# Optimization experiments

Hardware: AMD Instinct MI355X
Metric: run time of the kernel (lower is better)

Reference implementation:

```python
import jax, jax.numpy as jnp
import numpy as np

B = 256      # graphs per batch
N_PER = 256  # nodes per graph
DEG = 16     # avg degree
F_IN = 128   # num_feats
H = 128      # nhid
C = 10       # num_classes
RATIO = 0.5
N = B * N_PER
E = B * N_PER * DEG
K1 = int(np.ceil(RATIO * N_PER))   # 128
K2 = int(np.ceil(RATIO * K1))      # 64
K3 = int(np.ceil(RATIO * K2))      # 32


def setup_inputs() -> dict:
    key = jax.random.key(0)
    ks = jax.random.split(key, 24)
    off = (jnp.arange(B, dtype=jnp.int32) * N_PER)[:, None]
    # random intra-graph edges (block-diagonal adjacency)
    src = (jax.random.randint(ks[0], (B, N_PER * DEG), 0, N_PER, dtype=jnp.int32) + off).reshape(-1)
    dst = (jax.random.randint(ks[1], (B, N_PER * DEG), 0, N_PER, dtype=jnp.int32) + off).reshape(-1)
    x = jax.random.normal(ks[2], (N, F_IN), jnp.float32)

    def glorot(k, fi, fo):
        s = jnp.sqrt(2.0 / (fi + fo)).astype(jnp.float32)
        return jax.random.normal(k, (fi, fo), jnp.float32) * s

    inp = dict(x=x, src=src, dst=dst)
    # GCN conv layers
    inp['W1'] = glorot(ks[3], F_IN, H); inp['b1'] = jnp.zeros((H,), jnp.float32)
    inp['W2'] = glorot(ks[4], H, H);    inp['b2'] = jnp.zeros((H,), jnp.float32)
    inp['W3'] = glorot(ks[5], H, H);    inp['b3'] = jnp.zeros((H,), jnp.float32)
    # SAGPool score layers (GCNConv(nhid, 1))
    inp['Ws1'] = glorot(ks[6], H, 1); inp['bs1'] = jnp.zeros((1,), jnp.float32)
    inp['Ws2'] = glorot(ks[7], H, 1); inp['bs2'] = jnp.zeros((1,), jnp.float32)
    inp['Ws3'] = glorot(ks[8], H, 1); inp['bs3'] = jnp.zeros((1,), jnp.float32)
    # MLP head
    inp['Wl1'] = glorot(ks[9], 2 * H, H);      inp['bl1'] = jnp.zeros((H,), jnp.float32)
    inp['Wl2'] = glorot(ks[10], H, H // 2);    inp['bl2'] = jnp.zeros((H // 2,), jnp.float32)
    inp['Wl3'] = glorot(ks[11], H // 2, C);    inp['bl3'] = jnp.zeros((C,), jnp.float32)
    return inp


def _gcn(x, W, b, src, dst, mask):
    # PyG GCNConv: add self-loops, sym-normalize by deg^-1/2, aggregate x@W.
    # `mask` marks surviving nodes; edges with a dropped endpoint are inactive,
    # which is equivalent to PyG's filter_adj subgraph relabeling.
    emf = (mask[src] & mask[dst]).astype(x.dtype)           # [E]
    deg = jax.ops.segment_sum(emf, dst, num_segments=N) + mask.astype(x.dtype)  # +1 self loop
    dinv = jnp.where(deg > 0, jax.lax.rsqrt(deg), 0.0)
    h = x @ W                                                # [N, out]
    w = emf * dinv[src] * dinv[dst]                          # [E]
    agg = jax.ops.segment_sum(h[src] * w[:, None], dst, num_segments=N)
    agg = agg + h * (dinv * dinv * mask.astype(x.dtype))[:, None]  # self-loop term
    return agg + b


def _sagpool(x, Ws, bs, src, dst, mask, k):
    # score = GCNConv(in,1)(x); keep top-k per graph; x = x[perm]*tanh(score[perm])
    score = _gcn(x, Ws, bs, src, dst, mask)[:, 0]            # [N]
    s = jnp.where(mask, score, -jnp.inf).reshape(B, N_PER)
    idx = jax.lax.top_k(s, k)[1]                             # [B, k]
    nm = jnp.zeros((B, N_PER), bool).at[jnp.arange(B)[:, None], idx].set(True).reshape(-1)
    x = x * jnp.tanh(score)[:, None] * nm[:, None].astype(x.dtype)
    return x, nm


def _readout(x, mask, count):
    # global_max_pool || global_mean_pool over surviving nodes of each graph
    xb = x.reshape(B, N_PER, H)
    mb = mask.reshape(B, N_PER)[:, :, None]
    mx = jnp.max(jnp.where(mb, xb, -jnp.inf), axis=1)
    mn = jnp.sum(xb * mb.astype(x.dtype), axis=1) / jnp.asarray(count, x.dtype)
    return jnp.concatenate([mx, mn], axis=1)                 # [B, 2H]


def reference(x, src, dst, W1, b1, W2, b2, W3, b3, Ws1, bs1, Ws2, bs2, Ws3, bs3,
              Wl1, bl1, Wl2, bl2, Wl3, bl3):
    m0 = jnp.ones((N,), bool)
    h = jax.nn.relu(_gcn(x, W1, b1, src, dst, m0))
    h, m1 = _sagpool(h, Ws1, bs1, src, dst, m0, K1)
    r1 = _readout(h, m1, K1)
    h = jax.nn.relu(_gcn(h, W2, b2, src, dst, m1))
    h, m2 = _sagpool(h, Ws2, bs2, src, dst, m1, K2)
    r2 = _readout(h, m2, K2)
    h = jax.nn.relu(_gcn(h, W3, b3, src, dst, m2))
    h, m3 = _sagpool(h, Ws3, bs3, src, dst, m2, K3)
    r3 = _readout(h, m3, K3)
    z = r1 + r2 + r3                                         # [B, 2H]
    z = jax.nn.relu(z @ Wl1 + bl1)
    # dropout skipped (eval mode / training=False)
    z = jax.nn.relu(z @ Wl2 + bl2)
    return jax.nn.log_softmax(jax.nn.relu(z @ Wl3 + bl3), axis=-1)
```

## Files before the change

kernel.cpp:

```cpp
#include <hip/hip_runtime.h>
#include <math.h>

#define NGRAPH 256
#define NPG 256
#define HF 128
#define EPG 4096
#define EPG2 4352
#define FSTR 132
#define PSTR 136

typedef __attribute__((ext_vector_type(8))) short bf16x8;
typedef __attribute__((ext_vector_type(4))) float f32x4;

template<int N> struct IC { static constexpr int value = N; };
template<bool B> struct BC { static constexpr bool value = B; };

static __device__ __forceinline__ unsigned bcu(float f){ return __builtin_bit_cast(unsigned, f); }
static __device__ __forceinline__ float bcf(unsigned u){ return __builtin_bit_cast(float, u); }
static __device__ __forceinline__ unsigned rtn16(float f){
  unsigned u = bcu(f);
  return (u + 0x7FFFu + ((u >> 16) & 1u)) >> 16;
}

__global__ __launch_bounds__(256) void prep_wt(const float* __restrict__ W1,
                                               const float* __restrict__ W2,
                                               const float* __restrict__ W3,
                                               short* __restrict__ Wt) {
  int idx = blockIdx.x * 256 + threadIdx.x;
  int L = idx >> 14, r = idx & 16383;
  int k = r >> 7, n = r & 127;
  const float* W = (L == 0) ? W1 : (L == 1) ? W2 : W3;
  float w = W[k*128 + n];
  unsigned hi = rtn16(w);
  float lo = w - bcf(hi << 16);
  short* Whi = Wt + (size_t)L * 2 * 16384;
  short* Wlo = Whi + 16384;
  Whi[n*128 + k] = (short)hi;
  Wlo[n*128 + k] = (short)(bcu(lo) >> 16);
}

#define BSTEP(OK, OI, KKc, Jc) do { \
  bool iLess = ((tid & (Jc)) == 0); \
  bool descR = ((tid & (KKc)) == 0); \
  bool myFirst = (kf > (OK)) || (kf == (OK) && ki < (OI)); \
  bool keep = (iLess == descR) ? myFirst : !myFirst; \
  if (!keep) { kf = (OK); ki = (OI); } \
} while (0)

#define WAVE0_SCAN() do { \
  if (wid == 0) { \
    int b4 = lane*4; \
    int c0=cntA[b4+0], c1=cntA[b4+1], c2=cntA[b4+2], c3=cntA[b4+3]; \
    int tot = c0+c1+c2+c3; \
    int run = tot; \
    _Pragma("unroll") \
    for (int off=1; off<64; off<<=1) { \
      int u = __shfl_up(run, off); \
      run += (lane >= off) ? u : 0; \
    } \
    int st = run - tot; \
    rloc[b4+0]=(unsigned short)st; \
    rloc[b4+1]=(unsigned short)(st+c0); \
    rloc[b4+2]=(unsigned short)(st+c0+c1); \
    rloc[b4+3]=(unsigned short)(st+c0+c1+c2); \
    curA[b4+0]=st; curA[b4+1]=st+c0; curA[b4+2]=st+c0+c1; curA[b4+3]=st+c0+c1+c2; \
    if (lane == 63) rloc[NPG] = (unsigned short)run; \
  } \
} while (0)

__global__ __launch_bounds__(1024, 4)
void fused_net(
    const float* __restrict__ x,
    const int* __restrict__ srcI, const int* __restrict__ dstI,
    const short* __restrict__ WtAll,
    const float* __restrict__ b1, const float* __restrict__ Ws1, const float* __restrict__ bs1,
    const float* __restrict__ b2, const float* __restrict__ Ws2, const float* __restrict__ bs2,
    const float* __restrict__ b3, const float* __restrict__ Ws3, const float* __restrict__ bs3,
    const float* __restrict__ Wl1, const float* __restrict__ bl1,
    const float* __restrict__ Wl2, const float* __restrict__ bl2,
    const float* __restrict__ Wl3, const float* __restrict__ bl3,
    float* __restrict__ out)
{
  __shared__ __align__(16) short hpair[2][NPG*PSTR];
  __shared__ unsigned char colS[EPG2 + 8];
  __shared__ unsigned short rloc[NPG+2];
  __shared__ unsigned selM[8];
  __shared__ float dinv[NPG];
  __shared__ __align__(16) float bvec[HF];
  __shared__ __align__(16) float wsv[HF];
  __shared__ float score[NPG];
  __shared__ float tscale[NPG];
  __shared__ float skey[NPG];
  __shared__ int   sidx[NPG];
  __shared__ unsigned char rank8[NPG];
  __shared__ unsigned char lut[NPG];
  __shared__ __align__(16) float red[1024];
  __shared__ __align__(16) float red2[1024];
  __shared__ float zacc[2*HF];

  float* tbufF = (float*)&hpair[0][0];
  short* hp0 = &hpair[0][0];
  short* hp1 = &hpair[1][0];
  int* cntA = (int*)skey;
  int* curA = sidx;

  int tid = threadIdx.x;
  int g = blockIdx.x;
  size_t nbase = (size_t)g * NPG;
  int lane = tid & 63, wid = tid >> 6;

  const float4* X4 = (const float4*)(x + nbase*HF);
  #pragma unroll
  for (int i = 0; i < 8; ++i) {
    int f4 = tid + i*1024;
    int r = f4 >> 5, kq = f4 & 31;
    float4 val = X4[f4];
    unsigned rx = rtn16(val.x), ry = rtn16(val.y), rz = rtn16(val.z), rw = rtn16(val.w);
    uint2 ph; ph.x = rx | (ry << 16); ph.y = rz | (rw << 16);
    float lx = val.x - bcf(rx << 16), ly = val.y - bcf(ry << 16);
    float lz = val.z - bcf(rz << 16), lw = val.w - bcf(rw << 16);
    uint2 pl; pl.x = (bcu(lx) >> 16) | (bcu(ly) & 0xFFFF0000u);
    pl.y = (bcu(lz) >> 16) | (bcu(lw) & 0xFFFF0000u);
    *(uint2*)&hp0[r*PSTR + kq*4] = ph;
    *(uint2*)&hp1[r*PSTR + kq*4] = pl;
  }

  int nb = g * NPG;
  int dloc[4], sloc[4];
  #pragma unroll
  for (int it = 0; it < 4; ++it) {
    int e = g*EPG + tid + it*1024;
    dloc[it] = dstI[e] - nb;
    sloc[it] = srcI[e] - nb;
  }

  if (tid < NPG) { cntA[tid] = 1; lut[tid] = (unsigned char)tid; }
  __syncthreads();
  #pragma unroll
  for (int it = 0; it < 4; ++it) atomicAdd(&cntA[dloc[it]], 1);
  __syncthreads();
  WAVE0_SCAN();
  __syncthreads();
  #pragma unroll
  for (int it = 0; it < 4; ++it) {
    int slot = atomicAdd(&curA[dloc[it]], 1);
    colS[slot] = (unsigned char)sloc[it];
  }
  if (tid < NPG) colS[rloc[tid+1] - 1] = (unsigned char)tid;

  auto run_layer = [&](auto nrc, auto kc, auto firstc, auto packc,
                       const short* Whi, const short* Wlo,
                       const float* bias, const float* Wsc, const float* bscp) {
    constexpr int NR = decltype(nrc)::value;
    constexpr int K  = decltype(kc)::value;
    constexpr bool FIRST = decltype(firstc)::value;
    constexpr bool PACK  = decltype(packc)::value;
    constexpr int TPN = 1024 / NR;
    constexpr int NI  = 32 / TPN;
    constexpr int SH  = (TPN == 4) ? 2 : ((TPN == 8) ? 3 : 4);
    constexpr int RT  = NR / 64;
    int v = tid >> SH, q = tid & (TPN - 1);
    int cb0 = 4 * q;

    __syncthreads();

    if (tid < HF) { bvec[tid] = bias[tid]; wsv[tid] = Wsc[tid]; }
    if (tid < NR) dinv[tid] = 1.0f / sqrtf((float)((int)rloc[tid+1] - (int)rloc[tid]));

    {
      int rg = wid & 3, cg = wid >> 2;
      int lr = lane & 15, lk8 = (lane >> 4) * 8;
      f32x4 tacc[RT][2] = {};
      #pragma unroll
      for (int kc2 = 0; kc2 < 4; ++kc2) {
        int k0 = kc2*32 + lk8;
        bf16x8 ah[RT], al[RT];
        #pragma unroll
        for (int rt = 0; rt < RT; ++rt) {
          int row = rg*(NR/4) + rt*16 + lr;
          ah[rt] = *(const bf16x8*)&hp0[row*PSTR + k0];
          al[rt] = *(const bf16x8*)&hp1[row*PSTR + k0];
        }
        #pragma unroll
        for (int ct = 0; ct < 2; ++ct) {
          int n = cg*32 + ct*16 + lr;
          bf16x8 bh = *(const bf16x8*)&Whi[n*HF + k0];
          bf16x8 bl = *(const bf16x8*)&Wlo[n*HF + k0];
          #pragma unroll
          for (int rt = 0; rt < RT; ++rt) {
            tacc[rt][ct] = __builtin_amdgcn_mfma_f32_16x16x32_bf16(ah[rt], bh, tacc[rt][ct], 0, 0, 0);
            tacc[rt][ct] = __builtin_amdgcn_mfma_f32_16x16x32_bf16(al[rt], bh, tacc[rt][ct], 0, 0, 0);
            tacc[rt][ct] = __builtin_amdgcn_mfma_f32_16x16x32_bf16(ah[rt], bl, tacc[rt][ct], 0, 0, 0);
          }
        }
      }
      __syncthreads();
      #pragma unroll
      for (int rt = 0; rt < RT; ++rt) {
        int row0 = rg*(NR/4) + rt*16 + (lane >> 4)*4;
        float d0 = dinv[row0+0], d1 = dinv[row0+1], d2 = dinv[row0+2], d3 = dinv[row0+3];
        #pragma unroll
        for (int ct = 0; ct < 2; ++ct) {
          int c = cg*32 + ct*16 + (lane & 15);
          tbufF[(row0+0)*FSTR + c] = tacc[rt][ct][0] * d0;
          tbufF[(row0+1)*FSTR + c] = tacc[rt][ct][1] * d1;
          tbufF[(row0+2)*FSTR + c] = tacc[rt][ct][2] * d2;
          tbufF[(row0+3)*FSTR + c] = tacc[rt][ct][3] * d3;
        }
      }
    }
    __syncthreads();

    float4 hv[NI];
    {
      float4 acc[NI];
      #pragma unroll
      for (int j = 0; j < NI; ++j) { acc[j].x = acc[j].y = acc[j].z = acc[j].w = 0.f; }
      int e0 = rloc[v], e1 = rloc[v+1];
      int sA = colS[e0], sB = colS[e0+1], sC = colS[e0+2], sD = colS[e0+3];
      int e = e0;
      for (; e + 1 < e1; e += 2) {
        int s0 = sA, s1 = sB;
        sA = sC; sB = sD; sC = colS[e+4]; sD = colS[e+5];
        const float* g0 = &tbufF[s0*FSTR + cb0];
        const float* g1 = &tbufF[s1*FSTR + cb0];
        #pragma unroll
        for (int j = 0; j < NI; ++j) {
          float4 t0 = *(const float4*)&g0[j*4*TPN];
          float4 t1 = *(const float4*)&g1[j*4*TPN];
          acc[j].x += t0.x + t1.x; acc[j].y += t0.y + t1.y;
          acc[j].z += t0.z + t1.z; acc[j].w += t0.w + t1.w;
        }
      }
      if (e < e1) {
        const float* g0 = &tbufF[sA*FSTR + cb0];
        #pragma unroll
        for (int j = 0; j < NI; ++j) {
          float4 t0 = *(const float4*)&g0[j*4*TPN];
          acc[j].x += t0.x; acc[j].y += t0.y; acc[j].z += t0.z; acc[j].w += t0.w;
        }
      }
      float dv = dinv[v];
      float p = 0.f;
      #pragma unroll
      for (int j = 0; j < NI; ++j) {
        int ci = cb0 + j*4*TPN;
        float4 bv = *(const float4*)&bvec[ci];
        float4 wv = *(const float4*)&wsv[ci];
        float4 a;
        a.x = fmaxf(fmaf(dv, acc[j].x, bv.x), 0.f);
        a.y = fmaxf(fmaf(dv, acc[j].y, bv.y), 0.f);
        a.z = fmaxf(fmaf(dv, acc[j].z, bv.z), 0.f);
        a.w = fmaxf(fmaf(dv, acc[j].w, bv.w), 0.f);
        hv[j] = a;
        p += a.x*wv.x + a.y*wv.y + a.z*wv.z + a.w*wv.w;
      }
      red[tid] = p;
    }
    __syncthreads();
    if (tid < NR) {
      float s4 = 0.f;
      #pragma unroll
      for (int t = 0; t < TPN/4; ++t) {
        float4 qd = *(const float4*)&red[tid*TPN + 4*t];
        s4 += (qd.x + qd.y) + (qd.z + qd.w);
      }
      tscale[tid] = s4 * dinv[tid];
    }
    __syncthreads();
    if (tid < NR) {
      int e0 = rloc[tid], e1 = rloc[tid+1];
      float sa = 0.f;
      int sA = colS[e0], sB = colS[e0+1], sC = colS[e0+2], sD = colS[e0+3];
      for (int e = e0; e < e1; ++e) {
        int s = sA; sA = sB; sB = sC; sC = sD; sD = colS[e+4];
        sa += tscale[s];
      }
      score[tid] = dinv[tid] * sa + bscp[0];
    }
    __syncthreads();

    float kf = -INFINITY; int ki = tid;
    if (tid < NR) {
      kf = score[tid];
      for (int kk = 2; kk <= 64; kk <<= 1)
        for (int j = kk >> 1; j > 0; j >>= 1) {
          float ok = __shfl_xor(kf, j);
          int   oi = __shfl_xor(ki, j);
          BSTEP(ok, oi, kk, j);
        }
    } else if (tid < NR + 8) selM[tid - NR] = 0u;

    if constexpr (NR == 256) {
      if (tid < NR) { skey[tid] = kf; sidx[tid] = ki; }
      __syncthreads();
      if (tid < NR) {
        int l = tid ^ 64; float ok = skey[l]; int oi = sidx[l];
        BSTEP(ok, oi, 128, 64);
        for (int j = 32; j > 0; j >>= 1) {
          float sk = __shfl_xor(kf, j); int si = __shfl_xor(ki, j);
          BSTEP(sk, si, 128, j);
        }
      }
      __syncthreads();
      if (tid < NR) { skey[tid] = kf; sidx[tid] = ki; }
      __syncthreads();
      if (tid < NR) {
        int l = tid ^ 128; float ok = skey[l]; int oi = sidx[l];
        BSTEP(ok, oi, 256, 128);
      }
      __syncthreads();
      if (tid < NR) { skey[tid] = kf; sidx[tid] = ki; }
      __syncthreads();
      if (tid < NR) {
        int l = tid ^ 64; float ok = skey[l]; int oi = sidx[l];
        BSTEP(ok, oi, 256, 64);
        for (int j = 32; j > 0; j >>= 1) {
          float sk = __shfl_xor(kf, j); int si = __shfl_xor(ki, j);
          BSTEP(sk, si, 256, j);
        }
      }
    } else if constexpr (NR == 128) {
      if (tid < NR) { skey[tid] = kf; sidx[tid] = ki; }
      __syncthreads();
      if (tid < NR) {
        int l = tid ^ 64; float ok = skey[l]; int oi = sidx[l];
        BSTEP(ok, oi, 128, 64);
        for (int j = 32; j > 0; j >>= 1) {
          float sk = __shfl_xor(kf, j); int si = __shfl_xor(ki, j);
          BSTEP(sk, si, 128, j);
        }
      }
    }
    if constexpr (NR == 64) __syncthreads();
    if constexpr (NR != 64 && NR != 256) __syncthreads();
    if (tid < K) atomicOr(&selM[ki >> 5], 1u << (ki & 31));
    __syncthreads();

    if (tid < NR) {
      unsigned wsel = selM[tid >> 5];
      bool sel = (wsel >> (tid & 31)) & 1;
      int r = __popc(wsel & ((1u << (tid & 31)) - 1u));
      for (int w = 0; w < (tid >> 5); ++w) r += __popc(selM[w]);
      rank8[tid] = sel ? (unsigned char)r : (unsigned char)0xFF;
      tscale[tid] = sel ? tanhf(score[tid]) : 0.f;
    }
    __syncthreads();
    if (tid < NPG) {
      int lv = lut[tid];
      lut[tid] = (lv < NR) ? rank8[lv] : (unsigned char)0xFF;
    }

    int rk = rank8[v];
    {
      float ts = tscale[v];
      if (rk != 0xFF) {
        #pragma unroll
        for (int j = 0; j < NI; ++j) {
          hv[j].x *= ts; hv[j].y *= ts; hv[j].z *= ts; hv[j].w *= ts;
          *(float4*)&tbufF[rk*FSTR + cb0 + j*4*TPN] = hv[j];
        }
      }
    }
    __syncthreads();

    {
      constexpr int RPG = K / 8;
      int f = tid & 127, vg = tid >> 7;
      float mx = -INFINITY, sm = 0.f;
      #pragma unroll
      for (int vr = 0; vr < RPG; ++vr) {
        float val = tbufF[(vg*RPG + vr)*FSTR + f];
        mx = fmaxf(mx, val); sm += val;
      }
      red[vg*HF + f] = mx;
      red2[vg*HF + f] = sm;
      __syncthreads();
      if (tid < HF) {
        float zm = red[tid];
        float zs = red2[tid];
        #pragma unroll
        for (int q2 = 1; q2 < 8; ++q2) {
          zm = fmaxf(zm, red[q2*HF + tid]);
          zs += red2[q2*HF + tid];
        }
        float mn = zs / (float)K;
        if (FIRST) { zacc[tid] = zm; zacc[HF + tid] = mn; }
        else       { zacc[tid] += zm; zacc[HF + tid] += mn; }
      }
      __syncthreads();
    }

    if constexpr (PACK) {
      if (rk != 0xFF) {
        #pragma unroll
        for (int j = 0; j < NI; ++j) {
          int ci = cb0 + j*4*TPN;
          float4 val = hv[j];
          unsigned rx = rtn16(val.x), ry = rtn16(val.y), rz = rtn16(val.z), rw = rtn16(val.w);
          uint2 ph; ph.x = rx | (ry << 16); ph.y = rz | (rw << 16);
          float lx = val.x - bcf(rx << 16), ly = val.y - bcf(ry << 16);
          float lz = val.z - bcf(rz << 16), lw = val.w - bcf(rw << 16);
          uint2 pl; pl.x = (bcu(lx) >> 16) | (bcu(ly) & 0xFFFF0000u);
          pl.y = (bcu(lz) >> 16) | (bcu(lw) & 0xFFFF0000u);
          *(uint2*)&hp0[rk*PSTR + ci] = ph;
          *(uint2*)&hp1[rk*PSTR + ci] = pl;
        }
      }

      if (tid < K) cntA[tid] = 1; else if (tid < NPG) cntA[tid] = 0;
      __syncthreads();
      #pragma unroll
      for (int it = 0; it < 4; ++it) {
        int d2 = lut[dloc[it]], s2 = lut[sloc[it]];
        if (d2 < K && s2 < K) atomicAdd(&cntA[d2], 1);
      }
      __syncthreads();
      WAVE0_SCAN();
      __syncthreads();
      #pragma unroll
      for (int it = 0; it < 4; ++it) {
        int d2 = lut[dloc[it]], s2 = lut[sloc[it]];
        if (d2 < K && s2 < K) {
          int slot = atomicAdd(&curA[d2], 1);
          colS[slot] = (unsigned char)s2;
        }
      }
      if (tid < K) colS[rloc[tid+1] - 1] = (unsigned char)tid;
    }
  };

  run_layer(IC<256>{}, IC<128>{}, BC<true>{},  BC<true>{},
            WtAll,         WtAll + 16384, b1, Ws1, bs1);
  run_layer(IC<128>{}, IC<64>{},  BC<false>{}, BC<true>{},
            WtAll + 32768, WtAll + 49152, b2, Ws2, bs2);
  run_layer(IC<64>{},  IC<32>{},  BC<false>{}, BC<false>{},
            WtAll + 65536, WtAll + 81920, b3, Ws3, bs3);

  __syncthreads();

  {
    int o = tid & 127, kg = tid >> 7;
    float p = 0.f;
    int k0 = kg*32;
    for (int k = k0; k < k0+32; ++k) p += zacc[k]*Wl1[k*HF + o];
    red[kg*HF + o] = p;
    __syncthreads();
    if (tid < HF) {
      float a = bl1[tid];
      #pragma unroll
      for (int q2 = 0; q2 < 8; ++q2) a += red[q2*HF + tid];
      score[tid] = fmaxf(a, 0.f);
    }
    __syncthreads();
    if (tid < 512) {
      int o2 = tid & 63, kg2 = tid >> 6;
      float p2 = 0.f;
      int k0b = kg2*16;
      for (int k = k0b; k < k0b+16; ++k) p2 += score[k]*Wl2[k*64 + o2];
      red[kg2*64 + o2] = p2;
    }
    __syncthreads();
    if (tid < 64) {
      float a = bl2[tid];
      #pragma unroll
      for (int q2 = 0; q2 < 8; ++q2) a += red[q2*64 + tid];
      tscale[tid] = fmaxf(a, 0.f);
    }
    __syncthreads();
    if (tid < 10) {
      float a = bl3[tid];
      for (int k = 0; k < 64; ++k) a += tscale[k]*Wl3[k*10 + tid];
      dinv[tid] = fmaxf(a, 0.f);
    }
    __syncthreads();
    if (tid == 0) {
      float m = dinv[0];
      for (int i = 1; i < 10; ++i) m = fmaxf(m, dinv[i]);
      float s = 0.f;
      for (int i = 0; i < 10; ++i) s += expf(dinv[i] - m);
      red[0] = m; red[1] = logf(s);
    }
    __syncthreads();
    if (tid < 10) out[(size_t)g*10 + tid] = dinv[tid] - red[0] - red[1];
  }
}

extern "C" void kernel_launch(void* const* d_in, const int* in_sizes, int n_in,
                              void* d_out, int out_size, void* d_ws, size_t ws_size,
                              hipStream_t stream) {
  const float* x   = (const float*)d_in[0];
  const int*  srcI = (const int*)d_in[1];
  const int*  dstI = (const int*)d_in[2];
  const float* W1  = (const float*)d_in[3];
  const float* b1  = (const float*)d_in[4];
  const float* W2  = (const float*)d_in[5];
  const float* b2  = (const float*)d_in[6];
  const float* W3  = (const float*)d_in[7];
  const float* b3  = (const float*)d_in[8];
  const float* Ws1 = (const float*)d_in[9];
  const float* bs1 = (const float*)d_in[10];
  const float* Ws2 = (const float*)d_in[11];
  const float* bs2 = (const float*)d_in[12];
  const float* Ws3 = (const float*)d_in[13];
  const float* bs3 = (const float*)d_in[14];
  const float* Wl1 = (const float*)d_in[15];
  const float* bl1 = (const float*)d_in[16];
  const float* Wl2 = (const float*)d_in[17];
  const float* bl2 = (const float*)d_in[18];
  const float* Wl3 = (const float*)d_in[19];
  const float* bl3 = (const float*)d_in[20];
  float* out = (float*)d_out;

  short* WtAll = (short*)d_ws;

  prep_wt<<<192, 256, 0, stream>>>(W1, W2, W3, WtAll);
  fused_net<<<NGRAPH, 1024, 0, stream>>>(x, srcI, dstI, WtAll,
                                         b1, Ws1, bs1, b2, Ws2, bs2, b3, Ws3, bs3,
                                         Wl1, bl1, Wl2, bl2, Wl3, bl3, out);
}
```

Baseline: 84.07 us.

## Assign one wavefront per node for GCN aggregation and score propagation

The neighbor aggregation switches from a few threads per node, each covering column chunks, to a whole wavefront per node where each lane owns two feature columns. Edge indices are loaded cooperatively and broadcast with readlane. The score dot product and the score propagation now use wave shuffle reductions instead of LDS partial sums, which removes one barrier pass. The aim is to balance uneven-degree work and avoid the serialized per-node score loop, at the cost of sequential node loops per wave and narrower float2 LDS accesses.

```diff
diff --git a/kernel.cpp b/kernel.cpp
--- a/kernel.cpp
+++ b/kernel.cpp
@@ -155,12 +155,8 @@
     constexpr int K  = decltype(kc)::value;
     constexpr bool FIRST = decltype(firstc)::value;
     constexpr bool PACK  = decltype(packc)::value;
-    constexpr int TPN = 1024 / NR;
-    constexpr int NI  = 32 / TPN;
-    constexpr int SH  = (TPN == 4) ? 2 : ((TPN == 8) ? 3 : 4);
+    constexpr int NPW = NR / 16;
     constexpr int RT  = NR / 64;
-    int v = tid >> SH, q = tid & (TPN - 1);
-    int cb0 = 4 * q;
 
     __syncthreads();
 
@@ -211,72 +207,65 @@
     }
     __syncthreads();
 
-    float4 hv[NI];
+    float2 harr[NPW];
     {
-      float4 acc[NI];
-      #pragma unroll
-      for (int j = 0; j < NI; ++j) { acc[j].x = acc[j].y = acc[j].z = acc[j].w = 0.f; }
-      int e0 = rloc[v], e1 = rloc[v+1];
-      int sA = colS[e0], sB = colS[e0+1], sC = colS[e0+2], sD = colS[e0+3];
-      int e = e0;
-      for (; e + 1 < e1; e += 2) {
-        int s0 = sA, s1 = sB;
-        sA = sC; sB = sD; sC = colS[e+4]; sD = colS[e+5];
-        const float* g0 = &tbufF[s0*FSTR + cb0];
-        const float* g1 = &tbufF[s1*FSTR + cb0];
+      float2 bv2, wv2;
+      bv2.x = bvec[2*lane]; bv2.y = bvec[2*lane+1];
+      wv2.x = wsv[2*lane];  wv2.y = wsv[2*lane+1];
+      int lofs = 2*lane;
+      #pragma unroll
+      for (int nn = 0; nn < NPW; ++nn) {
+        int v = wid*NPW + nn;
+        int e0  = __builtin_amdgcn_readfirstlane((int)rloc[v]);
+        int len = __builtin_amdgcn_readfirstlane((int)rloc[v+1]) - e0;
+        float ax0 = 0.f, ay0 = 0.f, ax1 = 0.f, ay1 = 0.f;
+        for (int c = 0; c < len; c += 64) {
+          int rem = len - c;
+          int cc = rem < 64 ? rem : 64;
+          unsigned cv = (lane < cc) ? (unsigned)colS[e0 + c + lane] : 0u;
+          int k = 0;
+          for (; k + 1 < cc; k += 2) {
+            int s0 = __builtin_amdgcn_readlane((int)cv, k);
+            int s1 = __builtin_amdgcn_readlane((int)cv, k + 1);
+            float2 t0 = *(const float2*)&tbufF[s0*FSTR + lofs];
+            float2 t1 = *(const float2*)&tbufF[s1*FSTR + lofs];
+            ax0 += t0.x; ay0 += t0.y;
+            ax1 += t1.x; ay1 += t1.y;
+          }
+          if (k < cc) {
+            int s0 = __builtin_amdgcn_readlane((int)cv, k);
+            float2 t0 = *(const float2*)&tbufF[s0*FSTR + lofs];
+            ax0 += t0.x; ay0 += t0.y;
+          }
+        }
+        float dv = dinv[v];
+        float hx = fmaxf(fmaf(dv, ax0 + ax1, bv2.x), 0.f);
+        float hy = fmaxf(fmaf(dv, ay0 + ay1, bv2.y), 0.f);
+        harr[nn].x = hx; harr[nn].y = hy;
+        float p = hx*wv2.x + hy*wv2.y;
         #pragma unroll
-        for (int j = 0; j < NI; ++j) {
-          float4 t0 = *(const float4*)&g0[j*4*TPN];
-          float4 t1 = *(const float4*)&g1[j*4*TPN];
-          acc[j].x += t0.x + t1.x; acc[j].y += t0.y + t1.y;
-          acc[j].z += t0.z + t1.z; acc[j].w += t0.w + t1.w;
-        }
-      }
-      if (e < e1) {
-        const float* g0 = &tbufF[sA*FSTR + cb0];
+        for (int o = 32; o > 0; o >>= 1) p += __shfl_xor(p, o);
+        if (lane == 0) tscale[v] = p * dv;
+      }
+    }
+    __syncthreads();
+
+    {
+      float bsc = bscp[0];
+      #pragma unroll
+      for (int nn = 0; nn < NPW; ++nn) {
+        int v = wid*NPW + nn;
+        int e0  = __builtin_amdgcn_readfirstlane((int)rloc[v]);
+        int len = __builtin_amdgcn_readfirstlane((int)rloc[v+1]) - e0;
+        float t = 0.f;
+        for (int c = 0; c < len; c += 64) {
+          int rem = len - c;
+          if (lane < rem) t += tscale[colS[e0 + c + lane]];
+        }
         #pragma unroll
-        for (int j = 0; j < NI; ++j) {
-          float4 t0 = *(const float4*)&g0[j*4*TPN];
-          acc[j].x += t0.x; acc[j].y += t0.y; acc[j].z += t0.z; acc[j].w += t0.w;
-        }
-      }
-      float dv = dinv[v];
-      float p = 0.f;
-      #pragma unroll
-      for (int j = 0; j < NI; ++j) {
-        int ci = cb0 + j*4*TPN;
-        float4 bv = *(const float4*)&bvec[ci];
-        float4 wv = *(const float4*)&wsv[ci];
-        float4 a;
-        a.x = fmaxf(fmaf(dv, acc[j].x, bv.x), 0.f);
-        a.y = fmaxf(fmaf(dv, acc[j].y, bv.y), 0.f);
-        a.z = fmaxf(fmaf(dv, acc[j].z, bv.z), 0.f);
-        a.w = fmaxf(fmaf(dv, acc[j].w, bv.w), 0.f);
-        hv[j] = a;
-        p += a.x*wv.x + a.y*wv.y + a.z*wv.z + a.w*wv.w;
-      }
-      red[tid] = p;
-    }
-    __syncthreads();
-    if (tid < NR) {
-      float s4 = 0.f;
-      #pragma unroll
-      for (int t = 0; t < TPN/4; ++t) {
-        float4 qd = *(const float4*)&red[tid*TPN + 4*t];
-        s4 += (qd.x + qd.y) + (qd.z + qd.w);
-      }
-      tscale[tid] = s4 * dinv[tid];
-    }
-    __syncthreads();
-    if (tid < NR) {
-      int e0 = rloc[tid], e1 = rloc[tid+1];
-      float sa = 0.f;
-      int sA = colS[e0], sB = colS[e0+1], sC = colS[e0+2], sD = colS[e0+3];
-      for (int e = e0; e < e1; ++e) {
-        int s = sA; sA = sB; sB = sC; sC = sD; sD = colS[e+4];
-        sa += tscale[s];
-      }
-      score[tid] = dinv[tid] * sa + bscp[0];
+        for (int o = 32; o > 0; o >>= 1) t += __shfl_xor(t, o);
+        if (lane == 0) score[v] = dinv[v]*t + bsc;
+      }
     }
     __syncthreads();
 
@@ -332,8 +321,7 @@
         }
       }
     }
-    if constexpr (NR == 64) __syncthreads();
-    if constexpr (NR != 64 && NR != 256) __syncthreads();
+    __syncthreads();
     if (tid < K) atomicOr(&selM[ki >> 5], 1u << (ki & 31));
     __syncthreads();
 
@@ -351,15 +339,17 @@
       lut[tid] = (lv < NR) ? rank8[lv] : (unsigned char)0xFF;
     }
 
-    int rk = rank8[v];
     {
-      float ts = tscale[v];
-      if (rk != 0xFF) {
-        #pragma unroll
-        for (int j = 0; j < NI; ++j) {
-          hv[j].x *= ts; hv[j].y *= ts; hv[j].z *= ts; hv[j].w *= ts;
-          *(float4*)&tbufF[rk*FSTR + cb0 + j*4*TPN] = hv[j];
-        }
+      int lofs = 2*lane;
+      #pragma unroll
+      for (int nn = 0; nn < NPW; ++nn) {
+        int v = wid*NPW + nn;
+        int rk = rank8[v];
+        float ts = tscale[v];
+        float2 h = harr[nn];
+        h.x *= ts; h.y *= ts;
+        harr[nn] = h;
+        if (rk != 0xFF) *(float2*)&tbufF[rk*FSTR + lofs] = h;
       }
     }
     __syncthreads();
@@ -375,36 +365,35 @@
       }
       red[vg*HF + f] = mx;
       red2[vg*HF + f] = sm;
-      __syncthreads();
-      if (tid < HF) {
-        float zm = red[tid];
-        float zs = red2[tid];
+    }
+    __syncthreads();
+    if (tid < HF) {
+      float zm = red[tid];
+      float zs = red2[tid];
+      #pragma unroll
+      for (int q2 = 1; q2 < 8; ++q2) {
+        zm = fmaxf(zm, red[q2*HF + tid]);
+        zs += red2[q2*HF + tid];
+      }
+      float mn = zs / (float)K;
+      if (FIRST) { zacc[tid] = zm; zacc[HF + tid] = mn; }
+      else       { zacc[tid] += zm; zacc[HF + tid] += mn; }
+    }
+
+    if constexpr (PACK) {
+      {
+        int lofs = 2*lane;
         #pragma unroll
-        for (int q2 = 1; q2 < 8; ++q2) {
-          zm = fmaxf(zm, red[q2*HF + tid]);
-          zs += red2[q2*HF + tid];
-        }
-        float mn = zs / (float)K;
-        if (FIRST) { zacc[tid] = zm; zacc[HF + tid] = mn; }
-        else       { zacc[tid] += zm; zacc[HF + tid] += mn; }
-      }
-      __syncthreads();
-    }
-
-    if constexpr (PACK) {
-      if (rk != 0xFF) {
-        #pragma unroll
-        for (int j = 0; j < NI; ++j) {
-          int ci = cb0 + j*4*TPN;
-          float4 val = hv[j];
-          unsigned rx = rtn16(val.x), ry = rtn16(val.y), rz = rtn16(val.z), rw = rtn16(val.w);
-          uint2 ph; ph.x = rx | (ry << 16); ph.y = rz | (rw << 16);
-          float lx = val.x - bcf(rx << 16), ly = val.y - bcf(ry << 16);
-          float lz = val.z - bcf(rz << 16), lw = val.w - bcf(rw << 16);
-          uint2 pl; pl.x = (bcu(lx) >> 16) | (bcu(ly) & 0xFFFF0000u);
-          pl.y = (bcu(lz) >> 16) | (bcu(lw) & 0xFFFF0000u);
-          *(uint2*)&hp0[rk*PSTR + ci] = ph;
-          *(uint2*)&hp1[rk*PSTR + ci] = pl;
+        for (int nn = 0; nn < NPW; ++nn) {
+          int v = wid*NPW + nn;
+          int rk = rank8[v];
+          if (rk != 0xFF) {
+            float2 h = harr[nn];
+            unsigned rx = rtn16(h.x), ry = rtn16(h.y);
+            float lx = h.x - bcf(rx << 16), ly = h.y - bcf(ry << 16);
+            *(unsigned*)&hp0[rk*PSTR + lofs] = rx | (ry << 16);
+            *(unsigned*)&hp1[rk*PSTR + lofs] = (bcu(lx) >> 16) | (bcu(ly) & 0xFFFF0000u);
+          }
         }
       }
 
```

Result: slower. 100.9 us (+20.0%).

## Overlap CSR rebuild with layer phases to cut block barriers

Applied to the files above, without the earlier changes.

Moves the per-layer edge-count accumulation into the readout phase and the prefix scan plus column fill into the next layer's GEMM phase, so they share existing barriers. The separate synchronized rebuild block at the end of each layer goes away. dinv now comes from the count array rather than row-pointer differences. tanh of scores is computed by otherwise idle threads during the sort instead of after selection. This removes several __syncthreads per layer, but relies on subtle ordering between the scan, GEMM reads and the atomics, and the tscale change writes tanh for unselected nodes where the old code wrote zero.

```diff
diff --git a/kernel.cpp b/kernel.cpp
--- a/kernel.cpp
+++ b/kernel.cpp
@@ -148,13 +148,14 @@
   }
   if (tid < NPG) colS[rloc[tid+1] - 1] = (unsigned char)tid;
 
-  auto run_layer = [&](auto nrc, auto kc, auto firstc, auto packc,
+  auto run_layer = [&](auto nrc, auto kc, auto firstc, auto packc, auto buildc,
                        const short* Whi, const short* Wlo,
                        const float* bias, const float* Wsc, const float* bscp) {
     constexpr int NR = decltype(nrc)::value;
     constexpr int K  = decltype(kc)::value;
     constexpr bool FIRST = decltype(firstc)::value;
     constexpr bool PACK  = decltype(packc)::value;
+    constexpr bool BUILD = decltype(buildc)::value;
     constexpr int TPN = 1024 / NR;
     constexpr int NI  = 32 / TPN;
     constexpr int SH  = (TPN == 4) ? 2 : ((TPN == 8) ? 3 : 4);
@@ -165,7 +166,8 @@
     __syncthreads();
 
     if (tid < HF) { bvec[tid] = bias[tid]; wsv[tid] = Wsc[tid]; }
-    if (tid < NR) dinv[tid] = 1.0f / sqrtf((float)((int)rloc[tid+1] - (int)rloc[tid]));
+    if (tid < NR) dinv[tid] = 1.0f / sqrtf((float)cntA[tid]);
+    if constexpr (BUILD) WAVE0_SCAN();
 
     {
       int rg = wid & 3, cg = wid >> 2;
@@ -208,6 +210,17 @@
           tbufF[(row0+3)*FSTR + c] = tacc[rt][ct][3] * d3;
         }
       }
+    }
+    if constexpr (BUILD) {
+      #pragma unroll
+      for (int it = 0; it < 4; ++it) {
+        int d2 = lut[dloc[it]], s2 = lut[sloc[it]];
+        if (d2 < NR && s2 < NR) {
+          int slot = atomicAdd(&curA[d2], 1);
+          colS[slot] = (unsigned char)s2;
+        }
+      }
+      if (tid < NR) colS[rloc[tid+1] - 1] = (unsigned char)tid;
     }
     __syncthreads();
 
@@ -289,7 +302,11 @@
           int   oi = __shfl_xor(ki, j);
           BSTEP(ok, oi, kk, j);
         }
-    } else if (tid < NR + 8) selM[tid - NR] = 0u;
+    } else {
+      if (tid < NR + 8) selM[tid - NR] = 0u;
+      int vt = tid - NR;
+      if (vt < NR) tscale[vt] = tanhf(score[vt]);
+    }
 
     if constexpr (NR == 256) {
       if (tid < NR) { skey[tid] = kf; sidx[tid] = ki; }
@@ -343,7 +360,9 @@
       int r = __popc(wsel & ((1u << (tid & 31)) - 1u));
       for (int w = 0; w < (tid >> 5); ++w) r += __popc(selM[w]);
       rank8[tid] = sel ? (unsigned char)r : (unsigned char)0xFF;
-      tscale[tid] = sel ? tanhf(score[tid]) : 0.f;
+    }
+    if constexpr (PACK) {
+      if (tid < NPG) cntA[tid] = (tid < K) ? 1 : 0;
     }
     __syncthreads();
     if (tid < NPG) {
@@ -375,20 +394,26 @@
       }
       red[vg*HF + f] = mx;
       red2[vg*HF + f] = sm;
-      __syncthreads();
-      if (tid < HF) {
-        float zm = red[tid];
-        float zs = red2[tid];
-        #pragma unroll
-        for (int q2 = 1; q2 < 8; ++q2) {
-          zm = fmaxf(zm, red[q2*HF + tid]);
-          zs += red2[q2*HF + tid];
-        }
-        float mn = zs / (float)K;
-        if (FIRST) { zacc[tid] = zm; zacc[HF + tid] = mn; }
-        else       { zacc[tid] += zm; zacc[HF + tid] += mn; }
-      }
-      __syncthreads();
+    }
+    if constexpr (PACK) {
+      #pragma unroll
+      for (int it = 0; it < 4; ++it) {
+        int d2 = lut[dloc[it]], s2 = lut[sloc[it]];
+        if (d2 < K && s2 < K) atomicAdd(&cntA[d2], 1);
+      }
+    }
+    __syncthreads();
+    if (tid < HF) {
+      float zm = red[tid];
+      float zs = red2[tid];
+      #pragma unroll
+      for (int q2 = 1; q2 < 8; ++q2) {
+        zm = fmaxf(zm, red[q2*HF + tid]);
+        zs += red2[q2*HF + tid];
+      }
+      float mn = zs / (float)K;
+      if (FIRST) { zacc[tid] = zm; zacc[HF + tid] = mn; }
+      else       { zacc[tid] += zm; zacc[HF + tid] += mn; }
     }
 
     if constexpr (PACK) {
@@ -407,34 +432,14 @@
           *(uint2*)&hp1[rk*PSTR + ci] = pl;
         }
       }
-
-      if (tid < K) cntA[tid] = 1; else if (tid < NPG) cntA[tid] = 0;
-      __syncthreads();
-      #pragma unroll
-      for (int it = 0; it < 4; ++it) {
-        int d2 = lut[dloc[it]], s2 = lut[sloc[it]];
-        if (d2 < K && s2 < K) atomicAdd(&cntA[d2], 1);
-      }
-      __syncthreads();
-      WAVE0_SCAN();
-      __syncthreads();
-      #pragma unroll
-      for (int it = 0; it < 4; ++it) {
-        int d2 = lut[dloc[it]], s2 = lut[sloc[it]];
-        if (d2 < K && s2 < K) {
-          int slot = atomicAdd(&curA[d2], 1);
-          colS[slot] = (unsigned char)s2;
-        }
-      }
-      if (tid < K) colS[rloc[tid+1] - 1] = (unsigned char)tid;
     }
   };
 
-  run_layer(IC<256>{}, IC<128>{}, BC<true>{},  BC<true>{},
+  run_layer(IC<256>{}, IC<128>{}, BC<true>{},  BC<true>{},  BC<false>{},
             WtAll,         WtAll + 16384, b1, Ws1, bs1);
-  run_layer(IC<128>{}, IC<64>{},  BC<false>{}, BC<true>{},
+  run_layer(IC<128>{}, IC<64>{},  BC<false>{}, BC<true>{},  BC<true>{},
             WtAll + 32768, WtAll + 49152, b2, Ws2, bs2);
-  run_layer(IC<64>{},  IC<32>{},  BC<false>{}, BC<false>{},
+  run_layer(IC<64>{},  IC<32>{},  BC<false>{}, BC<false>{}, BC<true>{},
             WtAll + 65536, WtAll + 81920, b3, Ws3, bs3);
 
   __syncthreads();
```

Result: no change. 82.52 us (-1.8%).
